# Kernel tuning notes

Measured on AMD Instinct MI355X. Metric: run time of the kernel, lower is better.

The kernel has to match this reference:

```python
import jax, jax.numpy as jnp
import numpy as np

B, T, N, D = 128, 5, 64, 4
F1, F2 = 32, 32            # cnn filters
H = 128                    # mlp hidden units
PRED_STEPS = 8

# fully-connected adjacency without self-loops (fc_matrix)
_adj = np.ones((N, N)) - np.eye(N)
SRC, TGT = np.where(_adj)
SRC = jnp.asarray(SRC)
TGT = jnp.asarray(TGT)
E = int(SRC.shape[0])      # N*(N-1) = 4032


def _glorot(key, shape):
    fan_in = shape[-2] if len(shape) >= 2 else shape[0]
    return jax.random.normal(key, shape, jnp.float32) * float(1.0 / np.sqrt(fan_in))


def setup_inputs() -> dict:
    key = jax.random.key(0)
    ks = jax.random.split(key, 16)
    inp = {
        'time_segs': jax.random.normal(ks[0], (B, T, N, D), jnp.float32),
        # Conv1D over time: two valid convs, kernel 3
        'cw1': _glorot(ks[1], (3, D, F1)), 'cb1': jnp.zeros((F1,), jnp.float32),
        'cw2': _glorot(ks[2], (3, F1, F2)), 'cb2': jnp.zeros((F2,), jnp.float32),
        # edge encoder MLP: 2*F2 -> H -> H
        'ew1': _glorot(ks[3], (2 * F2, H)), 'eb1': jnp.zeros((H,), jnp.float32),
        'ew2': _glorot(ks[4], (H, H)), 'eb2': jnp.zeros((H,), jnp.float32),
        # node encoder MLP: H -> H -> H
        'nw1': _glorot(ks[5], (H, H)), 'nb1': jnp.zeros((H,), jnp.float32),
        'nw2': _glorot(ks[6], (H, H)), 'nb2': jnp.zeros((H,), jnp.float32),
        # node decoder MLP: (D + H) -> H -> H
        'dw1': _glorot(ks[7], (D + H, H)), 'db1': jnp.zeros((H,), jnp.float32),
        'dw2': _glorot(ks[8], (H, H)), 'db2': jnp.zeros((H,), jnp.float32),
        # output dense: H -> D
        'ow': _glorot(ks[9], (H, D)), 'ob': jnp.zeros((D,), jnp.float32),
    }
    return inp


def _mlp(x, w1, b1, w2, b2):
    h = jax.nn.relu(x @ w1 + b1)
    return jax.nn.relu(h @ w2 + b2)


def _conv_time(x, w, b):
    # x: [B, N, t, C]; valid conv (kernel 3) over time axis, relu
    b_, n_, t_, c_ = x.shape
    y = jax.lax.conv_general_dilated(
        x.reshape(b_ * n_, t_, c_), w, window_strides=(1,), padding='VALID',
        dimension_numbers=('NWC', 'WIO', 'NWC'))
    y = jax.nn.relu(y + b)
    return y.reshape(b_, n_, y.shape[1], y.shape[2])


def reference(time_segs, cw1, cb1, cw2, cb2, ew1, eb1, ew2, eb2,
              nw1, nb1, nw2, nb2, dw1, db1, dw2, db2, ow, ob):
    # [B, T, N, D] -> [B, N, T, D]
    window = jnp.transpose(time_segs, (0, 2, 1, 3))
    preds = []
    for _ in range(PRED_STEPS):
        # condense time: [B, N, 5, D] -> [B, N, 1, F2]
        h = _conv_time(window, cw1, cb1)
        h = _conv_time(h, cw2, cb2)
        # gather source/target node states per edge -> [B, E, 1, 2*F2]
        edge_in = jnp.concatenate([h[:, SRC], h[:, TGT]], axis=-1)
        edge_msg = _mlp(edge_in, ew1, eb1, ew2, eb2)           # [B, E, 1, H]
        # scatter-sum edge messages to target nodes -> [B, N, 1, H]
        node_msg = jnp.zeros((window.shape[0], N, 1, edge_msg.shape[-1]),
                             edge_msg.dtype).at[:, TGT].add(edge_msg)
        node_msg = _mlp(node_msg, nw1, nb1, nw2, nb2)
        prev = window[:, :, -1:, :]                            # [B, N, 1, D]
        dec = _mlp(jnp.concatenate([prev, node_msg], axis=-1), dw1, db1, dw2, db2)
        nxt = dec @ ow + ob + prev                             # residual, [B, N, 1, D]
        preds.append(nxt)
        window = jnp.concatenate([window[:, :, 1:, :], nxt], axis=2)
    out = jnp.concatenate(preds, axis=2)                       # [B, N, P, D]
    return jnp.transpose(out, (0, 2, 1, 3))                    # [B, P, N, D]
```

## Files before the change

kernel.cpp:

```cpp
#include <hip/hip_runtime.h>

#define WROW 52
#define TG 16

typedef _Float16 half_t;
typedef _Float16 half8 __attribute__((ext_vector_type(8)));
typedef float f32x4 __attribute__((ext_vector_type(4)));

#define SC 0.0009765625f

__device__ __forceinline__ unsigned pkrtz(float a, float b) {
  auto v = __builtin_amdgcn_cvt_pkrtz(a, b);
  return *(unsigned*)&v;
}

template<int LANES>
__device__ __forceinline__ void conv_proj(
    int lane, int gid, float* cp,
    const float* __restrict__ cw1, const float* __restrict__ cb1,
    const float* __restrict__ cw2, const float* __restrict__ cb2,
    const float* __restrict__ ew1,
    float* __restrict__ an, float* __restrict__ bn)
{
  #pragma unroll
  for (int o = 0; o < 96 / LANES; ++o) {
    int idx = lane + o * LANES;
    int tt = idx >> 5, f = idx & 31;
    float a = cb1[f];
    #pragma unroll
    for (int kt = 0; kt < 3; ++kt)
      #pragma unroll
      for (int d = 0; d < 4; ++d)
        a = fmaf(cp[(tt + kt) * 4 + d], cw1[(kt * 4 + d) * 32 + f], a);
    cp[32 + idx] = fmaxf(a, 0.f);
  }
  __syncthreads();
  #pragma unroll
  for (int o = 0; o < 32 / LANES; ++o) {
    int f = lane + o * LANES;
    float a = cb2[f];
    #pragma unroll
    for (int kt = 0; kt < 3; ++kt)
      for (int f1 = 0; f1 < 32; ++f1)
        a = fmaf(cp[32 + kt * 32 + f1], cw2[(kt * 32 + f1) * 32 + f], a);
    cp[128 + f] = fmaxf(a, 0.f);
  }
  __syncthreads();
  #pragma unroll
  for (int o = 0; o < 128 / LANES; ++o) {
    int j = lane + o * LANES;
    float a = 0.f, bb = 0.f;
    for (int f = 0; f < 32; ++f) {
      float h = cp[128 + f];
      a  = fmaf(h, ew1[f * 128 + j], a);
      bb = fmaf(h, ew1[(32 + f) * 128 + j], bb);
    }
    an[gid * 128 + j] = a * SC;
    bn[gid * 128 + j] = bb * SC;
  }
}

__global__ __launch_bounds__(256) void k_init(
    const float* __restrict__ ts,
    const float* __restrict__ cw1, const float* __restrict__ cb1,
    const float* __restrict__ cw2, const float* __restrict__ cb2,
    const float* __restrict__ ew1,
    float* __restrict__ win, float* __restrict__ an, float* __restrict__ bn)
{
  __shared__ float cp[16 * 160];
  int blk = blockIdx.x;
  int b = blk >> 2, n0 = (blk & 3) << 4;
  int tid = threadIdx.x;
  int ln = tid >> 4, lane = tid & 15;
  int n = n0 + ln;
  int gid = b * 64 + n;
  float* mycp = cp + ln * 160;
  for (int idx = lane; idx < 20; idx += 16) {
    int tt = idx >> 2, d = idx & 3;
    float v = ts[((b * 5 + tt) * 64 + n) * 4 + d];
    mycp[idx] = v;
    win[gid * WROW + idx] = v;
  }
  __syncthreads();
  conv_proj<16>(lane, gid, mycp, cw1, cb1, cw2, cb2, ew1, an, bn);
}

__global__ __launch_bounds__(256) void k_wsplit(
    const float* __restrict__ ew2, const float* __restrict__ nw1,
    const float* __restrict__ nw2, const float* __restrict__ dw1,
    const float* __restrict__ dw2, half_t* __restrict__ dst)
{
  int mat = blockIdx.x >> 6;
  const float* src = (mat == 0) ? ew2 : (mat == 1) ? nw1 : (mat == 2) ? nw2
                   : (mat == 3) ? (dw1 + 512) : dw2;
  half_t* dh = dst + mat * 2 * 16384;
  half_t* dl = dh + 16384;
  int g = (blockIdx.x & 63) * 256 + threadIdx.x;
  int k = g >> 7, col = g & 127;
  float x = src[g];
  _Float16 hi = (_Float16)x;
  float lo = x - (float)hi;
  int c = col >> 4, kb = k >> 5, kk = k & 31;
  int lane = ((kk >> 3) << 4) | (col & 15);
  int j = kk & 7;
  int idx = ((c * 4 + kb) * 64 + lane) * 8 + j;
  dh[idx] = hi;
  dl[idx] = (_Float16)lo;
}

__global__ __launch_bounds__(256, 2) void k_edge_v4(
    const float* __restrict__ an, const float* __restrict__ bn,
    const float* __restrict__ eb1, const float* __restrict__ eb2,
    const half_t* __restrict__ Bh, const half_t* __restrict__ Bl,
    float* __restrict__ nm)
{
  __shared__ __align__(16) half_t sAh[2][8192];
  __shared__ __align__(16) half_t sAl[2][8192];
  __shared__ float s_bt[TG * 128];
  int blk = blockIdx.x;
  int b = blk & 127, t0 = (blk >> 7) * TG;
  int tid = threadIdx.x;
  int w = tid >> 6, lane = tid & 63;

  #pragma unroll
  for (int i = 0; i < TG * 128 / 256; ++i) {
    int idx = tid + (i << 8);
    int tt = idx >> 7, j = idx & 127;
    s_bt[idx] = bn[((b << 6) + t0 + tt) * 128 + j] + eb1[j] * SC;
  }

  float au[4][8];
  {
    int kb8 = tid >> 4, sl = tid & 15;
    #pragma unroll
    for (int it = 0; it < 4; ++it) {
      const float* ap = an + (b << 13) + ((it * 16 + sl) << 7) + (kb8 << 3);
      float4 x0 = *(const float4*)ap;
      float4 x1 = *(const float4*)(ap + 4);
      au[it][0] = x0.x; au[it][1] = x0.y; au[it][2] = x0.z; au[it][3] = x0.w;
      au[it][4] = x1.x; au[it][5] = x1.y; au[it][6] = x1.z; au[it][7] = x1.w;
    }
  }

  half8 rbh[2][4], rbl[2][4];
  #pragma unroll
  for (int cc = 0; cc < 2; ++cc)
    #pragma unroll
    for (int kb = 0; kb < 4; ++kb) {
      int c = w * 2 + cc;
      rbh[cc][kb] = *(const half8*)(Bh + ((c * 4 + kb) * 64 + lane) * 8);
      rbl[cc][kb] = *(const half8*)(Bl + ((c * 4 + kb) * 64 + lane) * 8);
    }

  float bias0 = eb2[(w * 2 + 0) * 16 + (lane & 15)];
  float bias1 = eb2[(w * 2 + 1) * 16 + (lane & 15)];

  auto do_split = [&](int tt, half_t* dh, half_t* dl) {
    const float* bp = s_bt + (tt << 7) + ((tid >> 4) << 3);
    float4 b0 = *(const float4*)bp;
    float4 b1 = *(const float4*)(bp + 4);
    float bs[8] = {b0.x, b0.y, b0.z, b0.w, b1.x, b1.y, b1.z, b1.w};
    #pragma unroll
    for (int it = 0; it < 4; ++it) {
      int u = tid + (it << 8);
      float h32[8], l32[8];
      #pragma unroll
      for (int i = 0; i < 8; ++i) {
        float x = fmaxf(au[it][i] + bs[i], 0.f);
        float h = __uint_as_float(__float_as_uint(x) & 0xffffe000u);
        h32[i] = h;
        l32[i] = x - h;
      }
      unsigned hw[4], lw[4];
      #pragma unroll
      for (int p = 0; p < 4; ++p) {
        hw[p] = pkrtz(h32[2 * p], h32[2 * p + 1]);
        lw[p] = pkrtz(l32[2 * p], l32[2 * p + 1]);
      }
      *(uint4*)(dh + u * 8) = make_uint4(hw[0], hw[1], hw[2], hw[3]);
      *(uint4*)(dl + u * 8) = make_uint4(lw[0], lw[1], lw[2], lw[3]);
    }
  };

  __syncthreads();
  do_split(0, sAh[0], sAl[0]);
  __syncthreads();

  for (int tt = 0; tt < TG; ++tt) {
    int p = tt & 1;
    if (tt + 1 < TG) do_split(tt + 1, sAh[p ^ 1], sAl[p ^ 1]);

    const half_t* ph = sAh[p];
    const half_t* pl = sAl[p];
    f32x4 acc[4][2];
    #pragma unroll
    for (int rr = 0; rr < 4; ++rr)
      #pragma unroll
      for (int cc = 0; cc < 2; ++cc)
        acc[rr][cc] = (f32x4){0.f, 0.f, 0.f, 0.f};

    #pragma unroll
    for (int kb = 0; kb < 4; ++kb) {
      half8 ah[4], al[4];
      #pragma unroll
      for (int rr = 0; rr < 4; ++rr) {
        ah[rr] = *(const half8*)(ph + ((rr * 4 + kb) * 64 + lane) * 8);
        al[rr] = *(const half8*)(pl + ((rr * 4 + kb) * 64 + lane) * 8);
      }
      #pragma unroll
      for (int cc = 0; cc < 2; ++cc)
        #pragma unroll
        for (int rr = 0; rr < 4; ++rr) {
          acc[rr][cc] = __builtin_amdgcn_mfma_f32_16x16x32_f16(ah[rr], rbh[cc][kb], acc[rr][cc], 0, 0, 0);
          acc[rr][cc] = __builtin_amdgcn_mfma_f32_16x16x32_f16(ah[rr], rbl[cc][kb], acc[rr][cc], 0, 0, 0);
          acc[rr][cc] = __builtin_amdgcn_mfma_f32_16x16x32_f16(al[rr], rbh[cc][kb], acc[rr][cc], 0, 0, 0);
        }
    }

    int t = t0 + tt;
    float csum0 = 0.f, csum1 = 0.f;
    int rowoff = (lane >> 4) * 4;
    #pragma unroll
    for (int rr = 0; rr < 4; ++rr) {
      int sbase = rr * 16 + rowoff;
      #pragma unroll
      for (int q = 0; q < 4; ++q) {
        int s = sbase + q;
        float y0 = acc[rr][0][q] * 1024.f + bias0;
        float y1 = acc[rr][1][q] * 1024.f + bias1;
        if (s != t) {
          csum0 += fmaxf(y0, 0.f);
          csum1 += fmaxf(y1, 0.f);
        }
      }
    }
    csum0 += __shfl_xor(csum0, 16, 64);
    csum0 += __shfl_xor(csum0, 32, 64);
    csum1 += __shfl_xor(csum1, 16, 64);
    csum1 += __shfl_xor(csum1, 32, 64);
    if (lane < 32)
      nm[((b << 6) + t) * 128 + w * 32 + lane] = (lane < 16) ? csum0 : csum1;
    __syncthreads();
  }
}

__global__ __launch_bounds__(256) void k_nd_mfma(
    int step,
    const float* __restrict__ nm,
    const half_t* __restrict__ wsp,
    const float* __restrict__ nb1, const float* __restrict__ nb2,
    const float* __restrict__ dw1, const float* __restrict__ db1,
    const float* __restrict__ db2,
    const float* __restrict__ ow,  const float* __restrict__ ob,
    const float* __restrict__ cw1, const float* __restrict__ cb1,
    const float* __restrict__ cw2, const float* __restrict__ cb2,
    const float* __restrict__ ew1,
    float* __restrict__ win, float* __restrict__ an, float* __restrict__ bn,
    float* __restrict__ out)
{
  __shared__ __align__(16) float Xraw[16][132];
  __shared__ __align__(16) half_t sAh[2048];
  __shared__ __align__(16) half_t sAl[2048];
  __shared__ float sP[16][4];
  __shared__ float s_dw1a[4 * 128];
  __shared__ float s_nxt[16][4];
  __shared__ float cp[16 * 160];

  int blk = blockIdx.x;
  int b = blk >> 2, n0 = (blk & 3) << 4;
  int tid = threadIdx.x;
  int w = tid >> 6, lane = tid & 63;

  #pragma unroll
  for (int i = 0; i < 2; ++i) {
    int idx = tid + (i << 8);
    int row = idx >> 5, jf = idx & 31;
    *(float4*)&Xraw[row][jf << 2] =
        *(const float4*)(nm + ((b * 64 + n0 + row) << 7) + (jf << 2));
  }
  if (tid < 64) {
    int ln = tid >> 2, d = tid & 3;
    sP[ln][d] = win[(b * 64 + n0 + ln) * WROW + (step + 4) * 4 + d];
  }
  for (int idx = tid; idx < 512; idx += 256) s_dw1a[idx] = dw1[idx];
  __syncthreads();

  auto splitX = [&]() {
    int kb = tid >> 6, l = tid & 63;
    int row = l & 15, k0 = (kb << 5) + ((l >> 4) << 3);
    float h32[8], l32[8];
    #pragma unroll
    for (int i = 0; i < 8; ++i) {
      float x = Xraw[row][k0 + i] * SC;
      float h = __uint_as_float(__float_as_uint(x) & 0xffffe000u);
      h32[i] = h;
      l32[i] = x - h;
    }
    unsigned hw[4], lw[4];
    #pragma unroll
    for (int p = 0; p < 4; ++p) {
      hw[p] = pkrtz(h32[2 * p], h32[2 * p + 1]);
      lw[p] = pkrtz(l32[2 * p], l32[2 * p + 1]);
    }
    *(uint4*)(sAh + tid * 8) = make_uint4(hw[0], hw[1], hw[2], hw[3]);
    *(uint4*)(sAl + tid * 8) = make_uint4(lw[0], lw[1], lw[2], lw[3]);
  };

  auto layerM = [&](const half_t* Wh, const half_t* Wl,
                    const float* bias, bool withP) {
    splitX();
    __syncthreads();
    #pragma unroll
    for (int cc = 0; cc < 2; ++cc) {
      int c = w * 2 + cc;
      int col = c * 16 + (lane & 15);
      int row0 = (lane >> 4) * 4;
      float bj = bias[col];
      f32x4 acc;
      #pragma unroll
      for (int q = 0; q < 4; ++q) {
        float v = bj;
        if (withP) {
          #pragma unroll
          for (int d = 0; d < 4; ++d)
            v = fmaf(sP[row0 + q][d], s_dw1a[d * 128 + col], v);
        }
        acc[q] = v * SC;
      }
      #pragma unroll
      for (int kb = 0; kb < 4; ++kb) {
        half8 ah = *(const half8*)(sAh + ((kb << 6) + lane) * 8);
        half8 al = *(const half8*)(sAl + ((kb << 6) + lane) * 8);
        half8 bh = *(const half8*)(Wh + ((c * 4 + kb) * 64 + lane) * 8);
        half8 bl = *(const half8*)(Wl + ((c * 4 + kb) * 64 + lane) * 8);
        acc = __builtin_amdgcn_mfma_f32_16x16x32_f16(ah, bh, acc, 0, 0, 0);
        acc = __builtin_amdgcn_mfma_f32_16x16x32_f16(ah, bl, acc, 0, 0, 0);
        acc = __builtin_amdgcn_mfma_f32_16x16x32_f16(al, bh, acc, 0, 0, 0);
      }
      #pragma unroll
      for (int q = 0; q < 4; ++q)
        Xraw[row0 + q][col] = fmaxf(acc[q] * 1024.f, 0.f);
    }
    __syncthreads();
  };

  const half_t* nh1 = wsp + 2 * 16384;  const half_t* nl1 = nh1 + 16384;
  const half_t* nh2 = wsp + 4 * 16384;  const half_t* nl2 = nh2 + 16384;
  const half_t* dh1 = wsp + 6 * 16384;  const half_t* dl1 = dh1 + 16384;
  const half_t* dh2 = wsp + 8 * 16384;  const half_t* dl2 = dh2 + 16384;

  layerM(nh1, nl1, nb1, false);
  layerM(nh2, nl2, nb2, false);
  layerM(dh1, dl1, db1, true);
  layerM(dh2, dl2, db2, false);

  {
    int ln = tid >> 4, d = (tid >> 2) & 3, kq = tid & 3;
    float cs = 0.f;
    #pragma unroll
    for (int i = 0; i < 32; ++i) {
      int k = (kq << 5) + i;
      cs = fmaf(Xraw[ln][k], ow[k * 4 + d], cs);
    }
    cs += __shfl_xor(cs, 1, 64);
    cs += __shfl_xor(cs, 2, 64);
    if ((tid & 3) == 0) {
      float a = cs + ob[d] + sP[ln][d];
      int n = n0 + ln, gid = b * 64 + n;
      win[gid * WROW + (step + 5) * 4 + d] = a;
      out[((b * 8 + step) * 64 + n) * 4 + d] = a;
      s_nxt[ln][d] = a;
    }
  }
  __syncthreads();

  if (step < 7) {
    int ln = tid >> 4, lane2 = tid & 15;
    int gid = b * 64 + n0 + ln;
    float* mycp = cp + ln * 160;
    mycp[lane2] = win[gid * WROW + (step + 1) * 4 + lane2];
    if (lane2 < 4) mycp[16 + lane2] = s_nxt[ln][lane2];
    __syncthreads();
    conv_proj<16>(lane2, gid, mycp, cw1, cb1, cw2, cb2, ew1, an, bn);
  }
}

extern "C" void kernel_launch(void* const* d_in, const int* in_sizes, int n_in,
                              void* d_out, int out_size, void* d_ws, size_t ws_size,
                              hipStream_t stream) {
  (void)in_sizes; (void)n_in; (void)out_size; (void)ws_size;
  const float* ts  = (const float*)d_in[0];
  const float* cw1 = (const float*)d_in[1];
  const float* cb1 = (const float*)d_in[2];
  const float* cw2 = (const float*)d_in[3];
  const float* cb2 = (const float*)d_in[4];
  const float* ew1 = (const float*)d_in[5];
  const float* eb1 = (const float*)d_in[6];
  const float* ew2 = (const float*)d_in[7];
  const float* eb2 = (const float*)d_in[8];
  const float* nw1 = (const float*)d_in[9];
  const float* nb1 = (const float*)d_in[10];
  const float* nw2 = (const float*)d_in[11];
  const float* nb2 = (const float*)d_in[12];
  const float* dw1 = (const float*)d_in[13];
  const float* db1 = (const float*)d_in[14];
  const float* dw2 = (const float*)d_in[15];
  const float* db2 = (const float*)d_in[16];
  const float* ow  = (const float*)d_in[17];
  const float* ob  = (const float*)d_in[18];
  float* out = (float*)d_out;
  float* ws  = (float*)d_ws;
  float* win = ws;
  float* an  = win + 425984;
  float* bn  = an + 1048576;
  float* nmb = bn + 1048576;
  half_t* wsp = (half_t*)(nmb + 1048576);
  half_t* Bh = wsp;
  half_t* Bl = Bh + 16384;

  hipLaunchKernelGGL(k_wsplit, dim3(320), dim3(256), 0, stream,
                     ew2, nw1, nw2, dw1, dw2, wsp);
  hipLaunchKernelGGL(k_init, dim3(512), dim3(256), 0, stream,
                     ts, cw1, cb1, cw2, cb2, ew1, win, an, bn);
  for (int k = 0; k < 8; ++k) {
    hipLaunchKernelGGL(k_edge_v4, dim3(512), dim3(256), 0, stream,
                       an, bn, eb1, eb2, Bh, Bl, nmb);
    hipLaunchKernelGGL(k_nd_mfma, dim3(512), dim3(256), 0, stream,
                       k, nmb, wsp, nb1, nb2, dw1, db1, db2,
                       ow, ob, cw1, cb1, cw2, cb2, ew1, win, an, bn, out);
  }
}
```

Before: 565.6 us.

## Build edge MFMA A-fragments in registers and stage low-weight split in LDS

The edge kernel no longer writes the relu'd, hi/lo-split A operand into double-buffered shared memory. Each wave now holds its own copy of the source-node projection in registers, laid out to match the MFMA A fragment, and rebuilds the split fragments for every target row directly before the MFMAs. This removes the per-iteration LDS stores and loads and the block-wide barrier inside the loop. The low half of the weight split moves from registers to shared memory to offset the register cost. The trade-off is that every wave repeats the split arithmetic (4x redundant across waves) and holds 128 extra floats per thread, which raises register pressure and may cut occupancy.

```diff
diff --git a/kernel.cpp b/kernel.cpp
--- a/kernel.cpp
+++ b/kernel.cpp
@@ -108,15 +108,14 @@
   dl[idx] = (_Float16)lo;
 }
 
-__global__ __launch_bounds__(256, 2) void k_edge_v4(
+__global__ __launch_bounds__(256, 2) void k_edge_v5(
     const float* __restrict__ an, const float* __restrict__ bn,
     const float* __restrict__ eb1, const float* __restrict__ eb2,
     const half_t* __restrict__ Bh, const half_t* __restrict__ Bl,
     float* __restrict__ nm)
 {
-  __shared__ __align__(16) half_t sAh[2][8192];
-  __shared__ __align__(16) half_t sAl[2][8192];
   __shared__ float s_bt[TG * 128];
+  __shared__ __align__(16) half_t s_bl[16384];
   int blk = blockIdx.x;
   int b = blk & 127, t0 = (blk >> 7) * TG;
   int tid = threadIdx.x;
@@ -128,70 +127,46 @@
     int tt = idx >> 7, j = idx & 127;
     s_bt[idx] = bn[((b << 6) + t0 + tt) * 128 + j] + eb1[j] * SC;
   }
-
-  float au[4][8];
+  #pragma unroll
+  for (int i = 0; i < 8; ++i) {
+    int idx = tid + (i << 8);
+    ((uint4*)s_bl)[idx] = ((const uint4*)Bl)[idx];
+  }
+
+  float au[4][4][8];
   {
-    int kb8 = tid >> 4, sl = tid & 15;
-    #pragma unroll
-    for (int it = 0; it < 4; ++it) {
-      const float* ap = an + (b << 13) + ((it * 16 + sl) << 7) + (kb8 << 3);
-      float4 x0 = *(const float4*)ap;
-      float4 x1 = *(const float4*)(ap + 4);
-      au[it][0] = x0.x; au[it][1] = x0.y; au[it][2] = x0.z; au[it][3] = x0.w;
-      au[it][4] = x1.x; au[it][5] = x1.y; au[it][6] = x1.z; au[it][7] = x1.w;
-    }
-  }
-
-  half8 rbh[2][4], rbl[2][4];
+    int row16 = lane & 15, koff = (lane >> 4) << 3;
+    #pragma unroll
+    for (int rr = 0; rr < 4; ++rr)
+      #pragma unroll
+      for (int kb = 0; kb < 4; ++kb) {
+        const float* ap = an + (b << 13) + (((rr << 4) + row16) << 7)
+                        + (kb << 5) + koff;
+        float4 x0 = *(const float4*)ap;
+        float4 x1 = *(const float4*)(ap + 4);
+        au[rr][kb][0] = x0.x; au[rr][kb][1] = x0.y;
+        au[rr][kb][2] = x0.z; au[rr][kb][3] = x0.w;
+        au[rr][kb][4] = x1.x; au[rr][kb][5] = x1.y;
+        au[rr][kb][6] = x1.z; au[rr][kb][7] = x1.w;
+      }
+  }
+
+  half8 rbh[2][4];
   #pragma unroll
   for (int cc = 0; cc < 2; ++cc)
     #pragma unroll
     for (int kb = 0; kb < 4; ++kb) {
       int c = w * 2 + cc;
       rbh[cc][kb] = *(const half8*)(Bh + ((c * 4 + kb) * 64 + lane) * 8);
-      rbl[cc][kb] = *(const half8*)(Bl + ((c * 4 + kb) * 64 + lane) * 8);
     }
 
   float bias0 = eb2[(w * 2 + 0) * 16 + (lane & 15)];
   float bias1 = eb2[(w * 2 + 1) * 16 + (lane & 15)];
-
-  auto do_split = [&](int tt, half_t* dh, half_t* dl) {
-    const float* bp = s_bt + (tt << 7) + ((tid >> 4) << 3);
-    float4 b0 = *(const float4*)bp;
-    float4 b1 = *(const float4*)(bp + 4);
-    float bs[8] = {b0.x, b0.y, b0.z, b0.w, b1.x, b1.y, b1.z, b1.w};
-    #pragma unroll
-    for (int it = 0; it < 4; ++it) {
-      int u = tid + (it << 8);
-      float h32[8], l32[8];
-      #pragma unroll
-      for (int i = 0; i < 8; ++i) {
-        float x = fmaxf(au[it][i] + bs[i], 0.f);
-        float h = __uint_as_float(__float_as_uint(x) & 0xffffe000u);
-        h32[i] = h;
-        l32[i] = x - h;
-      }
-      unsigned hw[4], lw[4];
-      #pragma unroll
-      for (int p = 0; p < 4; ++p) {
-        hw[p] = pkrtz(h32[2 * p], h32[2 * p + 1]);
-        lw[p] = pkrtz(l32[2 * p], l32[2 * p + 1]);
-      }
-      *(uint4*)(dh + u * 8) = make_uint4(hw[0], hw[1], hw[2], hw[3]);
-      *(uint4*)(dl + u * 8) = make_uint4(lw[0], lw[1], lw[2], lw[3]);
-    }
-  };
-
-  __syncthreads();
-  do_split(0, sAh[0], sAl[0]);
+  int rowoff = (lane >> 4) * 4;
+
   __syncthreads();
 
   for (int tt = 0; tt < TG; ++tt) {
-    int p = tt & 1;
-    if (tt + 1 < TG) do_split(tt + 1, sAh[p ^ 1], sAl[p ^ 1]);
-
-    const half_t* ph = sAh[p];
-    const half_t* pl = sAl[p];
     f32x4 acc[4][2];
     #pragma unroll
     for (int rr = 0; rr < 4; ++rr)
@@ -201,25 +176,47 @@
 
     #pragma unroll
     for (int kb = 0; kb < 4; ++kb) {
+      const float* bp = s_bt + (tt << 7) + (kb << 5) + ((lane >> 4) << 3);
+      float4 b0 = *(const float4*)bp;
+      float4 b1 = *(const float4*)(bp + 4);
+      float bs[8] = {b0.x, b0.y, b0.z, b0.w, b1.x, b1.y, b1.z, b1.w};
+
       half8 ah[4], al[4];
       #pragma unroll
       for (int rr = 0; rr < 4; ++rr) {
-        ah[rr] = *(const half8*)(ph + ((rr * 4 + kb) * 64 + lane) * 8);
-        al[rr] = *(const half8*)(pl + ((rr * 4 + kb) * 64 + lane) * 8);
-      }
-      #pragma unroll
-      for (int cc = 0; cc < 2; ++cc)
+        float h32[8], l32[8];
+        #pragma unroll
+        for (int i = 0; i < 8; ++i) {
+          float x = fmaxf(au[rr][kb][i] + bs[i], 0.f);
+          float h = __uint_as_float(__float_as_uint(x) & 0xffffe000u);
+          h32[i] = h;
+          l32[i] = x - h;
+        }
+        union { unsigned u[4]; half8 h; } rh, rl;
+        #pragma unroll
+        for (int p = 0; p < 4; ++p) {
+          rh.u[p] = pkrtz(h32[2 * p], h32[2 * p + 1]);
+          rl.u[p] = pkrtz(l32[2 * p], l32[2 * p + 1]);
+        }
+        ah[rr] = rh.h;
+        al[rr] = rl.h;
+      }
+
+      #pragma unroll
+      for (int cc = 0; cc < 2; ++cc) {
+        int c = w * 2 + cc;
+        half8 bl = *(const half8*)(s_bl + ((c * 4 + kb) * 64 + lane) * 8);
         #pragma unroll
         for (int rr = 0; rr < 4; ++rr) {
           acc[rr][cc] = __builtin_amdgcn_mfma_f32_16x16x32_f16(ah[rr], rbh[cc][kb], acc[rr][cc], 0, 0, 0);
-          acc[rr][cc] = __builtin_amdgcn_mfma_f32_16x16x32_f16(ah[rr], rbl[cc][kb], acc[rr][cc], 0, 0, 0);
+          acc[rr][cc] = __builtin_amdgcn_mfma_f32_16x16x32_f16(ah[rr], bl, acc[rr][cc], 0, 0, 0);
           acc[rr][cc] = __builtin_amdgcn_mfma_f32_16x16x32_f16(al[rr], rbh[cc][kb], acc[rr][cc], 0, 0, 0);
         }
+      }
     }
 
     int t = t0 + tt;
     float csum0 = 0.f, csum1 = 0.f;
-    int rowoff = (lane >> 4) * 4;
     #pragma unroll
     for (int rr = 0; rr < 4; ++rr) {
       int sbase = rr * 16 + rowoff;
@@ -240,7 +237,6 @@
     csum1 += __shfl_xor(csum1, 32, 64);
     if (lane < 32)
       nm[((b << 6) + t) * 128 + w * 32 + lane] = (lane < 16) ? csum0 : csum1;
-    __syncthreads();
   }
 }
 
@@ -423,7 +419,7 @@
   hipLaunchKernelGGL(k_init, dim3(512), dim3(256), 0, stream,
                      ts, cw1, cb1, cw2, cb2, ew1, win, an, bn);
   for (int k = 0; k < 8; ++k) {
-    hipLaunchKernelGGL(k_edge_v4, dim3(512), dim3(256), 0, stream,
+    hipLaunchKernelGGL(k_edge_v5, dim3(512), dim3(256), 0, stream,
                        an, bn, eb1, eb2, Bh, Bl, nmb);
     hipLaunchKernelGGL(k_nd_mfma, dim3(512), dim3(256), 0, stream,
                        k, nmb, wsp, nb1, nb2, dw1, db1, db2,
```

Measured after the change: 745.5 us. 31.8% more time.
